# Optimization experiments

Hardware: AMD Instinct MI355X
Metric: run time of the kernel (lower is better)

The kernel has to match this reference:

```python
import jax, jax.numpy as jnp
import numpy as np

B, IN, OUT = 65536, 256, 256
EPS = 1e-10


def setup_inputs() -> dict:
    key = jax.random.key(0)
    k1, k2, k3 = jax.random.split(key, 3)
    x = jax.random.normal(k1, (B, IN), dtype=jnp.float32)
    # match nn.Linear default init scale roughly (kaiming-uniform-ish)
    W = jax.random.normal(k2, (OUT, IN), dtype=jnp.float32) / np.sqrt(IN)
    b = jax.random.normal(k3, (OUT,), dtype=jnp.float32) / np.sqrt(IN)
    return {"x": x, "W": W, "b": b}


def reference(x, W, b):
    # x: [B, in], W: [out, in], b: [out]
    # x_len[i] = sqrt(sum_k x[i,k]^2)  (original does x^2 @ ones^T -> same value per out col)
    x_len = jnp.sqrt(jnp.sum(x * x, axis=-1, keepdims=True))           # [B, 1]
    # w_len[j] = sqrt(sum_k W[j,k]^2)  (original does ones @ (W^2)^T -> same value per row)
    w_len = jnp.sqrt(jnp.sum(W * W, axis=-1))[None, :]                  # [1, out]
    x_len = jax.lax.stop_gradient(x_len)
    w_len = jax.lax.stop_gradient(w_len)
    b_sg = jax.lax.stop_gradient(b)
    out = x @ W.T + b                                                   # linear(x), grads flow
    out = out - b_sg[None, :]                                           # bias.data subtraction (no grad)
    out = jnp.maximum(out / (x_len * w_len), EPS)                       # cosine normalize + clamp
    out = out + b_sg[None, :]                                           # bias.data added back (no grad)
    return out
```

## Files before the change

### kernel.cpp

```cpp
#include <hip/hip_runtime.h>
#include <hip/hip_bf16.h>
#include <math.h>


using bf16x8 = __attribute__((ext_vector_type(8))) short;
using f32x4  = __attribute__((ext_vector_type(4))) float;

#define W_LDS_BYTES 131072
#define LDS_BYTES   (W_LDS_BYTES + 1024 + 1024)
#define EPS 1e-10f

__device__ __forceinline__ short f2bf(float f) {
    __bf16 h = (__bf16)f;
    return __builtin_bit_cast(short, h);
}

__global__ __launch_bounds__(1024, 4) void ffn_cosnorm_kernel(
    const float* __restrict__ x, const float* __restrict__ W,
    const float* __restrict__ b, float* __restrict__ out)
{
    extern __shared__ char smem[];
    float* winv = (float*)(smem + W_LDS_BYTES);
    float* blds = (float*)(smem + W_LDS_BYTES + 1024);

    const int t    = threadIdx.x;
    const int lane = t & 63;
    const int wave = t >> 6;
    const int r16  = lane & 15;
    const int kg   = lane >> 4;
    const int rxor = (r16 & 7) << 4;
    const size_t rowb = (size_t)blockIdx.x * 256 + (size_t)wave * 16;

    const float* xp = x + (rowb + r16) * 256 + kg * 8;

    float4 fa[8], fb[8];
    #pragma unroll
    for (int s = 0; s < 8; ++s) {
        fa[s] = *(const float4*)(xp + s * 32);
        fb[s] = *(const float4*)(xp + s * 32 + 4);
    }

    if (wave < 8) {
        const int wrow = t >> 1;
        const int half = t & 1;
        const float* wr = W + (size_t)wrow * 256 + half * 128;
        const int rx = (wrow & 7) << 4;
        float ss = 0.f;
        #pragma unroll
        for (int i = 0; i < 16; ++i) {
            float4 a = *(const float4*)(wr + i * 8);
            float4 c = *(const float4*)(wr + i * 8 + 4);
            ss = fmaf(a.x, a.x, ss); ss = fmaf(a.y, a.y, ss);
            ss = fmaf(a.z, a.z, ss); ss = fmaf(a.w, a.w, ss);
            ss = fmaf(c.x, c.x, ss); ss = fmaf(c.y, c.y, ss);
            ss = fmaf(c.z, c.z, ss); ss = fmaf(c.w, c.w, ss);
            bf16x8 v;
            v[0] = f2bf(a.x); v[1] = f2bf(a.y); v[2] = f2bf(a.z); v[3] = f2bf(a.w);
            v[4] = f2bf(c.x); v[5] = f2bf(c.y); v[6] = f2bf(c.z); v[7] = f2bf(c.w);
            const int off = wrow * 512 + ((half * 256 + i * 16) ^ rx);
            *(bf16x8*)(smem + off) = v;
        }
        ss += __shfl_xor(ss, 1);
        if (!half) winv[wrow] = 1.0f / sqrtf(ss);
        if (t < 256) blds[t] = b[t];
    }

    bf16x8 xb[8];
    float ssx = 0.f;
    #pragma unroll
    for (int s = 0; s < 8; ++s) {
        float4 a = fa[s], c = fb[s];
        bf16x8 v;
        v[0] = f2bf(a.x); v[1] = f2bf(a.y); v[2] = f2bf(a.z); v[3] = f2bf(a.w);
        v[4] = f2bf(c.x); v[5] = f2bf(c.y); v[6] = f2bf(c.z); v[7] = f2bf(c.w);
        xb[s] = v;
        ssx = fmaf(a.x, a.x, ssx); ssx = fmaf(a.y, a.y, ssx);
        ssx = fmaf(a.z, a.z, ssx); ssx = fmaf(a.w, a.w, ssx);
        ssx = fmaf(c.x, c.x, ssx); ssx = fmaf(c.y, c.y, ssx);
        ssx = fmaf(c.z, c.z, ssx); ssx = fmaf(c.w, c.w, ssx);
    }

    ssx += __shfl_xor(ssx, 16); ssx += __shfl_xor(ssx, 32);
    const float inv = 1.0f / sqrtf(ssx);

    __syncthreads();

    const int jb = kg * 4;
    float* op = out + (rowb + r16) * 256;

    #pragma unroll
    for (int n = 0; n < 16; ++n) {
        f32x4 acc = f32x4{0.f, 0.f, 0.f, 0.f};
        #pragma unroll
        for (int k0 = 0; k0 < 8; ++k0) {
            const int addr = (n * 16 + r16) * 512 + ((k0 * 64 + kg * 16) ^ rxor);
            bf16x8 wfr = *(const bf16x8*)(smem + addr);
            acc = __builtin_amdgcn_mfma_f32_16x16x32_bf16(wfr, xb[k0], acc, 0, 0, 0);
        }
        float4 wv = *(const float4*)(winv + n * 16 + jb);
        float4 bv = *(const float4*)(blds + n * 16 + jb);
        f32x4 o;
        o[0] = fmaxf(acc[0] * (inv * wv.x), EPS) + bv.x;
        o[1] = fmaxf(acc[1] * (inv * wv.y), EPS) + bv.y;
        o[2] = fmaxf(acc[2] * (inv * wv.z), EPS) + bv.z;
        o[3] = fmaxf(acc[3] * (inv * wv.w), EPS) + bv.w;
        *(f32x4*)(op + n * 16 + jb) = o;
    }
}

extern "C" void kernel_launch(void* const* d_in, const int* in_sizes, int n_in,
                              void* d_out, int out_size, void* d_ws, size_t ws_size,
                              hipStream_t stream) {
    const float* x = (const float*)d_in[0];
    const float* W = (const float*)d_in[1];
    const float* b = (const float*)d_in[2];
    float* out = (float*)d_out;

    hipFuncSetAttribute((const void*)ffn_cosnorm_kernel,
                        hipFuncAttributeMaxDynamicSharedMemorySize, LDS_BYTES);
    ffn_cosnorm_kernel<<<dim3(256), dim3(1024), LDS_BYTES, stream>>>(x, W, b, out);
}
```

Before: 34.64 us.

## Reorder GEMM loop k-outer and stream x chunks with double buffering

The loop order changes from n-outer/k-inner to k-outer/n-inner, with 16 accumulator tiles kept live in registers. The x row data now arrives in four chunks double-buffered in registers, so the global loads of later K chunks overlap the MFMA work on earlier ones instead of all 64 floats being loaded up front. The intent is to hide global load latency and reduce register pressure from the raw x buffer. In exchange it adds 64 accumulator registers and a sched_barrier, which may hurt occupancy or scheduling at 1024 threads per block.

```diff
diff --git a/kernel.cpp b/kernel.cpp
--- a/kernel.cpp
+++ b/kernel.cpp
@@ -13,6 +13,21 @@
 __device__ __forceinline__ short f2bf(float f) {
     __bf16 h = (__bf16)f;
     return __builtin_bit_cast(short, h);
+}
+
+__device__ __forceinline__ bf16x8 pack8(float4 a, float4 c) {
+    bf16x8 v;
+    v[0] = f2bf(a.x); v[1] = f2bf(a.y); v[2] = f2bf(a.z); v[3] = f2bf(a.w);
+    v[4] = f2bf(c.x); v[5] = f2bf(c.y); v[6] = f2bf(c.z); v[7] = f2bf(c.w);
+    return v;
+}
+
+__device__ __forceinline__ float sumsq8(float4 a, float4 c, float s) {
+    s = fmaf(a.x, a.x, s); s = fmaf(a.y, a.y, s);
+    s = fmaf(a.z, a.z, s); s = fmaf(a.w, a.w, s);
+    s = fmaf(c.x, c.x, s); s = fmaf(c.y, c.y, s);
+    s = fmaf(c.z, c.z, s); s = fmaf(c.w, c.w, s);
+    return s;
 }
 
 __global__ __launch_bounds__(1024, 4) void ffn_cosnorm_kernel(
@@ -33,11 +48,13 @@
 
     const float* xp = x + (rowb + r16) * 256 + kg * 8;
 
-    float4 fa[8], fb[8];
+    float4 qb[2][4];
     #pragma unroll
-    for (int s = 0; s < 8; ++s) {
-        fa[s] = *(const float4*)(xp + s * 32);
-        fb[s] = *(const float4*)(xp + s * 32 + 4);
+    for (int s = 0; s < 2; ++s) {
+        qb[s][0] = *(const float4*)(xp + (s * 2) * 32);
+        qb[s][1] = *(const float4*)(xp + (s * 2) * 32 + 4);
+        qb[s][2] = *(const float4*)(xp + (s * 2 + 1) * 32);
+        qb[s][3] = *(const float4*)(xp + (s * 2 + 1) * 32 + 4);
     }
 
     if (wave < 8) {
@@ -50,38 +67,19 @@
         for (int i = 0; i < 16; ++i) {
             float4 a = *(const float4*)(wr + i * 8);
             float4 c = *(const float4*)(wr + i * 8 + 4);
-            ss = fmaf(a.x, a.x, ss); ss = fmaf(a.y, a.y, ss);
-            ss = fmaf(a.z, a.z, ss); ss = fmaf(a.w, a.w, ss);
-            ss = fmaf(c.x, c.x, ss); ss = fmaf(c.y, c.y, ss);
-            ss = fmaf(c.z, c.z, ss); ss = fmaf(c.w, c.w, ss);
-            bf16x8 v;
-            v[0] = f2bf(a.x); v[1] = f2bf(a.y); v[2] = f2bf(a.z); v[3] = f2bf(a.w);
-            v[4] = f2bf(c.x); v[5] = f2bf(c.y); v[6] = f2bf(c.z); v[7] = f2bf(c.w);
+            ss = sumsq8(a, c, ss);
             const int off = wrow * 512 + ((half * 256 + i * 16) ^ rx);
-            *(bf16x8*)(smem + off) = v;
+            *(bf16x8*)(smem + off) = pack8(a, c);
         }
         ss += __shfl_xor(ss, 1);
         if (!half) winv[wrow] = 1.0f / sqrtf(ss);
         if (t < 256) blds[t] = b[t];
     }
 
-    bf16x8 xb[8];
+    f32x4 acc[16];
+    #pragma unroll
+    for (int n = 0; n < 16; ++n) acc[n] = f32x4{0.f, 0.f, 0.f, 0.f};
     float ssx = 0.f;
-    #pragma unroll
-    for (int s = 0; s < 8; ++s) {
-        float4 a = fa[s], c = fb[s];
-        bf16x8 v;
-        v[0] = f2bf(a.x); v[1] = f2bf(a.y); v[2] = f2bf(a.z); v[3] = f2bf(a.w);
-        v[4] = f2bf(c.x); v[5] = f2bf(c.y); v[6] = f2bf(c.z); v[7] = f2bf(c.w);
-        xb[s] = v;
-        ssx = fmaf(a.x, a.x, ssx); ssx = fmaf(a.y, a.y, ssx);
-        ssx = fmaf(a.z, a.z, ssx); ssx = fmaf(a.w, a.w, ssx);
-        ssx = fmaf(c.x, c.x, ssx); ssx = fmaf(c.y, c.y, ssx);
-        ssx = fmaf(c.z, c.z, ssx); ssx = fmaf(c.w, c.w, ssx);
-    }
-
-    ssx += __shfl_xor(ssx, 16); ssx += __shfl_xor(ssx, 32);
-    const float inv = 1.0f / sqrtf(ssx);
 
     __syncthreads();
 
@@ -89,22 +87,60 @@
     float* op = out + (rowb + r16) * 256;
 
     #pragma unroll
-    for (int n = 0; n < 16; ++n) {
-        f32x4 acc = f32x4{0.f, 0.f, 0.f, 0.f};
+    for (int q = 0; q < 3; ++q) {
+        const int s = q & 1;
+        float4 a0 = qb[s][0], c0 = qb[s][1], a1 = qb[s][2], c1 = qb[s][3];
+        bf16x8 f0 = pack8(a0, c0);
+        bf16x8 f1 = pack8(a1, c1);
+        ssx = sumsq8(a0, c0, ssx);
+        ssx = sumsq8(a1, c1, ssx);
+        if (q < 2) {
+            const float* p = xp + ((q + 2) * 2) * 32;
+            qb[s][0] = *(const float4*)(p);
+            qb[s][1] = *(const float4*)(p + 4);
+            qb[s][2] = *(const float4*)(p + 32);
+            qb[s][3] = *(const float4*)(p + 36);
+            __builtin_amdgcn_sched_barrier(0);
+        }
+        const int cs0 = ((q * 2) * 64 + kg * 16) ^ rxor;
+        const int cs1 = ((q * 2 + 1) * 64 + kg * 16) ^ rxor;
         #pragma unroll
-        for (int k0 = 0; k0 < 8; ++k0) {
-            const int addr = (n * 16 + r16) * 512 + ((k0 * 64 + kg * 16) ^ rxor);
-            bf16x8 wfr = *(const bf16x8*)(smem + addr);
-            acc = __builtin_amdgcn_mfma_f32_16x16x32_bf16(wfr, xb[k0], acc, 0, 0, 0);
+        for (int n = 0; n < 16; ++n) {
+            const int rowa = (n * 16 + r16) * 512;
+            bf16x8 w0 = *(const bf16x8*)(smem + rowa + cs0);
+            bf16x8 w1 = *(const bf16x8*)(smem + rowa + cs1);
+            acc[n] = __builtin_amdgcn_mfma_f32_16x16x32_bf16(w0, f0, acc[n], 0, 0, 0);
+            acc[n] = __builtin_amdgcn_mfma_f32_16x16x32_bf16(w1, f1, acc[n], 0, 0, 0);
         }
-        float4 wv = *(const float4*)(winv + n * 16 + jb);
-        float4 bv = *(const float4*)(blds + n * 16 + jb);
-        f32x4 o;
-        o[0] = fmaxf(acc[0] * (inv * wv.x), EPS) + bv.x;
-        o[1] = fmaxf(acc[1] * (inv * wv.y), EPS) + bv.y;
-        o[2] = fmaxf(acc[2] * (inv * wv.z), EPS) + bv.z;
-        o[3] = fmaxf(acc[3] * (inv * wv.w), EPS) + bv.w;
-        *(f32x4*)(op + n * 16 + jb) = o;
+    }
+
+    {
+        float4 a0 = qb[1][0], c0 = qb[1][1], a1 = qb[1][2], c1 = qb[1][3];
+        bf16x8 f0 = pack8(a0, c0);
+        bf16x8 f1 = pack8(a1, c1);
+        ssx = sumsq8(a0, c0, ssx);
+        ssx = sumsq8(a1, c1, ssx);
+        ssx += __shfl_xor(ssx, 16); ssx += __shfl_xor(ssx, 32);
+        const float inv = 1.0f / sqrtf(ssx);
+
+        const int cs0 = (6 * 64 + kg * 16) ^ rxor;
+        const int cs1 = (7 * 64 + kg * 16) ^ rxor;
+        #pragma unroll
+        for (int n = 0; n < 16; ++n) {
+            const int rowa = (n * 16 + r16) * 512;
+            bf16x8 w0 = *(const bf16x8*)(smem + rowa + cs0);
+            bf16x8 w1 = *(const bf16x8*)(smem + rowa + cs1);
+            f32x4 a = __builtin_amdgcn_mfma_f32_16x16x32_bf16(w0, f0, acc[n], 0, 0, 0);
+            a = __builtin_amdgcn_mfma_f32_16x16x32_bf16(w1, f1, a, 0, 0, 0);
+            float4 wv = *(const float4*)(winv + n * 16 + jb);
+            float4 bv = *(const float4*)(blds + n * 16 + jb);
+            f32x4 o;
+            o[0] = fmaxf(a[0] * (inv * wv.x), EPS) + bv.x;
+            o[1] = fmaxf(a[1] * (inv * wv.y), EPS) + bv.y;
+            o[2] = fmaxf(a[2] * (inv * wv.z), EPS) + bv.z;
+            o[3] = fmaxf(a[3] * (inv * wv.w), EPS) + bv.w;
+            *(f32x4*)(op + n * 16 + jb) = o;
+        }
     }
 }
 
```

After: 48.49 us. 40.0% more time.
